# Kernel optimization log

Measured on AMD Instinct MI355X. Metric: run time of the kernel, lower is better.

## Reference

```python
import jax, jax.numpy as jnp
import numpy as np

N_NODES = 50000
N_EDGES = 800000
IN_FEATS = 128
OUT_FEATS = 128
HEADS = 2
EW_DIMS = 2
NEG_SLOPE = 0.2


def setup_inputs() -> dict:
    key = jax.random.key(0)
    ks = jax.random.split(key, 8)
    feat = jax.random.normal(ks[0], (N_NODES, IN_FEATS), dtype=jnp.float32)
    e_w = jax.random.uniform(ks[1], (N_EDGES, EW_DIMS), dtype=jnp.float32)
    src = jax.random.randint(ks[2], (N_EDGES,), 0, N_NODES)
    dst = jax.random.randint(ks[3], (N_EDGES,), 0, N_NODES)
    # Learned params: per-head fc weight, attn vectors (xavier-ish scale)
    s = 1.0 / np.sqrt(IN_FEATS)
    W = jax.random.normal(ks[4], (HEADS, OUT_FEATS, IN_FEATS), dtype=jnp.float32) * s
    attn_l = jax.random.normal(ks[5], (HEADS, OUT_FEATS), dtype=jnp.float32) * s
    attn_r = jax.random.normal(ks[6], (HEADS, OUT_FEATS), dtype=jnp.float32) * s
    attn_ew = jax.random.normal(ks[7], (HEADS, EW_DIMS), dtype=jnp.float32)
    return {"feat": feat, "e_w": e_w, "src": src, "dst": dst,
            "W": W, "attn_l": attn_l, "attn_r": attn_r, "attn_ew": attn_ew}


def reference(feat, e_w, src, dst, W, attn_l, attn_r, attn_ew):
    N = feat.shape[0]
    # per-head projection: [N, H, O]
    ft = jnp.einsum('nf,hof->nho', feat, W)
    el = jnp.einsum('nho,ho->nh', ft, attn_l)           # [N, H]
    er = jnp.einsum('nho,ho->nh', ft, attn_r)           # [N, H]
    ew = jnp.einsum('ed,hd->eh', e_w, attn_ew)          # [E, H]
    # u_add_v + edge-weight attention + leaky_relu
    e = jax.nn.leaky_relu(el[src] + er[dst] + ew, NEG_SLOPE)  # [E, H]
    # edge_softmax grouped by destination node (numerically stable)
    emax = jax.ops.segment_max(e, dst, num_segments=N)
    emax = jnp.where(jnp.isfinite(emax), emax, 0.0)
    ee = jnp.exp(e - emax[dst])
    denom = jax.ops.segment_sum(ee, dst, num_segments=N)
    a = ee / jnp.where(denom[dst] > 0, denom[dst], 1.0)       # [E, H]
    # u_mul_e / sum aggregation: [N, H, O]
    m = ft[src] * a[:, :, None]
    rst = jax.ops.segment_sum(m, dst, num_segments=N)
    # residual (Identity since in_feats == out_feats) + elu, then cat heads
    rst = jax.nn.elu(rst + feat[:, None, :])
    return rst.reshape(N, -1)
```

## Files before the change

### kernel.cpp

```cpp
#include <hip/hip_runtime.h>
#include <math.h>

#define NNODES 50000
#define NEDGES 800000
#define INF 128
#define OUTF 128
#define HEADS 2
#define NEG_SLOPE 0.2f

#define NXCD 8
#define SCAPX 8
#define NSLOT 64
#define DCAP 32
#define OVFCAP 32768
#define OVFFLAG 0x40000000

__device__ __forceinline__ unsigned short f2bf(float f) {
    unsigned u = __float_as_uint(f);
    unsigned r = (u + 0x7FFFu + ((u >> 16) & 1u)) >> 16;
    return (unsigned short)r;
}
__device__ __forceinline__ float bf2f(unsigned short b) {
    return __uint_as_float((unsigned)b << 16);
}
__device__ __forceinline__ unsigned cvt_pk_bf16(float lo, float hi) {
    unsigned r;
    asm("v_cvt_pk_bf16_f32 %0, %1, %2" : "=v"(r) : "v"(lo), "v"(hi));
    return r;
}

typedef __attribute__((ext_vector_type(8))) short frag_ab;
typedef __attribute__((ext_vector_type(4))) float frag_cd;
typedef __attribute__((ext_vector_type(8))) unsigned short ushort8v;

#define APITCH 136

__global__ void init_kernel(int* cur8, int* ,
                            const float* __restrict__ W,
                            const float* __restrict__ attn_l,
                            const float* __restrict__ attn_r,
                            unsigned short* __restrict__ Wb,
                            float* __restrict__ wfold, int N) {
    const int b = blockIdx.x, t = threadIdx.x;
    const int zn = NXCD * N + 1;
    const int zblk = (zn + 255) >> 8;
    if (b < zblk) {
        int i = b * 256 + t;
        if (i < zn) cur8[i] = 0;
        return;
    }
    if (b == zblk) {
        int h = t >> 7, f = t & 127;
        float sl = 0.f, sr = 0.f;
#pragma unroll 16
        for (int o = 0; o < 128; ++o) {
            float wv = W[(size_t)(h * 128 + o) * 128 + f];
            sl = fmaf(attn_l[h * 128 + o], wv, sl);
            sr = fmaf(attn_r[h * 128 + o], wv, sr);
        }
        wfold[h * 128 + f] = sl;
        wfold[(2 + h) * 128 + f] = sr;
        return;
    }
    int base = (b - zblk - 1) * 4096 + t * 16;
#pragma unroll
    for (int q = 0; q < 4; ++q) {
        float4 g = *(const float4*)(W + base + q * 4);
        ushort4 v; v.x = f2bf(g.x); v.y = f2bf(g.y); v.z = f2bf(g.z); v.w = f2bf(g.w);
        *(ushort4*)(Wb + base + q * 4) = v;
    }
}

__global__ __launch_bounds__(256) void gemm_mfma(const float* __restrict__ feat,
                                                 const unsigned short* __restrict__ Wb,
                                                 const float* __restrict__ wfold,
                                                 unsigned short* __restrict__ ftb,
                                                 float* __restrict__ el,
                                                 float* __restrict__ er,
                                                 int N) {
    __shared__ unsigned short Bs[256 * APITCH];
    const int t = threadIdx.x;
    const int w = t >> 6, lane = t & 63;
    const int m16 = lane & 15, quad = lane >> 4;
    const int n0 = blockIdx.x * 128;
    const int r0 = n0 + w * 16 + m16;
    const int r1 = r0 + 64;
    const bool v0 = r0 < N, v1 = r1 < N;

#pragma unroll
    for (int i = 0; i < 16; ++i) {
        int q = t + i * 256;
        int row = q >> 4, c = q & 15;
        ushort8v v = *(const ushort8v*)(Wb + row * 128 + c * 8);
        *(ushort8v*)(&Bs[row * APITCH + c * 8]) = v;
    }

    frag_ab af[2][4];
    float pd[2][4] = {{0.f, 0.f, 0.f, 0.f}, {0.f, 0.f, 0.f, 0.f}};
#pragma unroll
    for (int kc = 0; kc < 4; ++kc) {
        const int cc = kc * 32 + quad * 8;
        float4 ga0 = make_float4(0.f, 0.f, 0.f, 0.f), ga1 = ga0;
        float4 gb0 = ga0, gb1 = ga0;
        if (v0) {
            ga0 = *(const float4*)(feat + (size_t)r0 * INF + cc);
            ga1 = *(const float4*)(feat + (size_t)r0 * INF + cc + 4);
        }
        if (v1) {
            gb0 = *(const float4*)(feat + (size_t)r1 * INF + cc);
            gb1 = *(const float4*)(feat + (size_t)r1 * INF + cc + 4);
        }
        union { int4 i; frag_ab f; } ua, ub;
        ua.i.x = (int)cvt_pk_bf16(ga0.x, ga0.y); ua.i.y = (int)cvt_pk_bf16(ga0.z, ga0.w);
        ua.i.z = (int)cvt_pk_bf16(ga1.x, ga1.y); ua.i.w = (int)cvt_pk_bf16(ga1.z, ga1.w);
        ub.i.x = (int)cvt_pk_bf16(gb0.x, gb0.y); ub.i.y = (int)cvt_pk_bf16(gb0.z, gb0.w);
        ub.i.z = (int)cvt_pk_bf16(gb1.x, gb1.y); ub.i.w = (int)cvt_pk_bf16(gb1.z, gb1.w);
        af[0][kc] = ua.f; af[1][kc] = ub.f;
#pragma unroll
        for (int vq = 0; vq < 4; ++vq) {
            float4 w0 = *(const float4*)(wfold + vq * 128 + cc);
            float4 w1 = *(const float4*)(wfold + vq * 128 + cc + 4);
            pd[0][vq] += ga0.x * w0.x + ga0.y * w0.y + ga0.z * w0.z + ga0.w * w0.w
                       + ga1.x * w1.x + ga1.y * w1.y + ga1.z * w1.z + ga1.w * w1.w;
            pd[1][vq] += gb0.x * w0.x + gb0.y * w0.y + gb0.z * w0.z + gb0.w * w0.w
                       + gb1.x * w1.x + gb1.y * w1.y + gb1.z * w1.z + gb1.w * w1.w;
        }
    }
#pragma unroll
    for (int m = 16; m < 64; m <<= 1)
#pragma unroll
        for (int rg = 0; rg < 2; ++rg)
#pragma unroll
            for (int vq = 0; vq < 4; ++vq) pd[rg][vq] += __shfl_xor(pd[rg][vq], m, 64);
    if (quad == 0) {
        if (v0) {
            *(float2*)(el + (size_t)r0 * 2) = make_float2(pd[0][0], pd[0][1]);
            *(float2*)(er + (size_t)r0 * 2) = make_float2(pd[0][2], pd[0][3]);
        }
        if (v1) {
            *(float2*)(el + (size_t)r1 * 2) = make_float2(pd[1][0], pd[1][1]);
            *(float2*)(er + (size_t)r1 * 2) = make_float2(pd[1][2], pd[1][3]);
        }
    }

    __syncthreads();

#pragma unroll 1
    for (int jt = 0; jt < 4; ++jt) {
        frag_cd acc[2][4];
#pragma unroll
        for (int rg = 0; rg < 2; ++rg)
#pragma unroll
            for (int nt = 0; nt < 4; ++nt) acc[rg][nt] = frag_cd{0.f, 0.f, 0.f, 0.f};
#pragma unroll
        for (int kc = 0; kc < 4; ++kc)
#pragma unroll
            for (int nt = 0; nt < 4; ++nt) {
                frag_ab bf = *(const frag_ab*)(&Bs[(jt * 64 + nt * 16 + m16) * APITCH
                                                   + kc * 32 + quad * 8]);
                acc[0][nt] = __builtin_amdgcn_mfma_f32_16x16x32_bf16(bf, af[0][kc],
                                                                     acc[0][nt], 0, 0, 0);
                acc[1][nt] = __builtin_amdgcn_mfma_f32_16x16x32_bf16(bf, af[1][kc],
                                                                     acc[1][nt], 0, 0, 0);
            }
#pragma unroll
        for (int rg = 0; rg < 2; ++rg) {
            const int rr = rg ? r1 : r0;
            if (rg ? v1 : v0) {
#pragma unroll
                for (int nt = 0; nt < 4; ++nt) {
                    uint2 p;
                    p.x = cvt_pk_bf16(acc[rg][nt][0], acc[rg][nt][1]);
                    p.y = cvt_pk_bf16(acc[rg][nt][2], acc[rg][nt][3]);
                    *(uint2*)(ftb + (size_t)rr * 256 + jt * 64 + nt * 16 + quad * 4) = p;
                }
            }
        }
    }
}

__global__ __launch_bounds__(256) void edge_fused(const float* __restrict__ el,
                           const float* __restrict__ er,
                           const float* __restrict__ e_w, const int* __restrict__ src,
                           const int* __restrict__ dst, const float* __restrict__ attn_ew,
                           int* __restrict__ cur8, int* __restrict__ ovfcnt,
                           uint2* __restrict__ bins, float4* __restrict__ ovf,
                           int E) {
    int e = blockIdx.x * 256 + threadIdx.x;
    if (e >= E) return;
    unsigned xcc;
    asm volatile("s_getreg_b32 %0, hwreg(HW_REG_XCC_ID)" : "=s"(xcc));
    xcc &= (NXCD - 1);
    int s = src[e], d = dst[e];
    float2 ew2 = *(const float2*)(e_w + (size_t)e * 2);
    float2 elv = *(const float2*)(el + (size_t)s * 2);
    float2 erv = *(const float2*)(er + (size_t)d * 2);
    float v0 = elv.x + erv.x + ew2.x * attn_ew[0] + ew2.y * attn_ew[1];
    float v1 = elv.y + erv.y + ew2.x * attn_ew[2] + ew2.y * attn_ew[3];
    v0 = v0 >= 0.f ? v0 : NEG_SLOPE * v0;
    v1 = v1 >= 0.f ? v1 : NEG_SLOPE * v1;
    float ee0 = __expf(v0);
    float ee1 = __expf(v1);
    int pos = __hip_atomic_fetch_add(cur8 + (size_t)d * NXCD + xcc, 1,
                                     __ATOMIC_RELAXED, __HIP_MEMORY_SCOPE_WORKGROUP);
    if (pos < SCAPX) {
        unsigned pk = ((unsigned)f2bf(ee1) << 16) | (unsigned)f2bf(ee0);
        bins[(size_t)d * NSLOT + xcc * SCAPX + pos] = make_uint2((unsigned)s, pk);
    } else {
        int o = atomicAdd(ovfcnt, 1);
        if (o < OVFCAP)
            ovf[o] = make_float4(__int_as_float(d), __int_as_float(s), ee0, ee1);
    }
}

__global__ __launch_bounds__(256) void compact_bins(uint2* __restrict__ bins,
                                                    const int* __restrict__ cur8,
                                                    int* __restrict__ cntd,
                                                    int* __restrict__ ovfcnt,
                                                    float4* __restrict__ ovf, int N) {
    const int t = threadIdx.x;
    const int w = t >> 6, l = t & 63;
    const int n = blockIdx.x * 4 + w;
    if (n >= N) return;
    const int x = l >> 3, slot = l & 7;
    const int cx = cur8[(size_t)n * NXCD + x];
    uint2 rec = bins[(size_t)n * NSLOT + l];
    const int cxc = cx < SCAPX ? cx : SCAPX;
    const bool valid = slot < cxc;
    unsigned long long mask = __ballot(valid);
    int pos = __popcll(mask & ((1ull << l) - 1ull));
    int tot = __popcll(mask);
    bool oflag = __any(slot == 0 && cx > SCAPX) || (tot > DCAP);
    if (valid) {
        if (pos < DCAP) {
            bins[(size_t)n * NSLOT + pos] = rec;
        } else {
            int o = atomicAdd(ovfcnt, 1);
            if (o < OVFCAP)
                ovf[o] = make_float4(__int_as_float(n), __int_as_float((int)rec.x),
                                     bf2f((unsigned short)(rec.y & 0xFFFFu)),
                                     bf2f((unsigned short)(rec.y >> 16)));
        }
    }
    if (l == 0) cntd[n] = (tot < DCAP ? tot : DCAP) | (oflag ? OVFFLAG : 0);
}

__global__ __launch_bounds__(256) void aggregate(const unsigned short* __restrict__ ftb,
                                                 const float* __restrict__ feat,
                                                 const uint2* __restrict__ bins,
                                                 const int* __restrict__ cntd,
                                                 const int* __restrict__ ovfcnt,
                                                 const float4* __restrict__ ovf,
                                                 float* __restrict__ out, int N) {
    const int t = threadIdx.x;
    const int w = t >> 6, l = t & 63;
    const int n = blockIdx.x * 4 + w;
    if (n >= N) return;
    const int hl = l & 31;
    const int half = l >> 5;
    const int c8 = 8 * hl;
    const int h = hl >> 4;
    const int cw = cntd[n];
    const int cnt = cw & 0xFFFF;
    const uint2* eb = bins + (size_t)n * NSLOT;

    float4 a0 = make_float4(0.f, 0.f, 0.f, 0.f);
    float4 a1 = make_float4(0.f, 0.f, 0.f, 0.f);
    float dn = 0.f;
    const int hm = (cnt + 1) >> 1;
#pragma unroll 8
    for (int i = 0; i < hm; ++i) {
        const int j = 2 * i + half;
        const bool vld = j < cnt;
        uint2 rec = eb[vld ? j : 0];
        float aw = bf2f((unsigned short)(h ? (rec.y >> 16) : (rec.y & 0xFFFFu)));
        float a = vld ? aw : 0.f;
        unsigned su = vld ? rec.x : 0u;
        ushort8v v = *(const ushort8v*)(ftb + (size_t)su * 256 + c8);
        dn += a;
        a0.x = fmaf(a, bf2f(v[0]), a0.x);
        a0.y = fmaf(a, bf2f(v[1]), a0.y);
        a0.z = fmaf(a, bf2f(v[2]), a0.z);
        a0.w = fmaf(a, bf2f(v[3]), a0.w);
        a1.x = fmaf(a, bf2f(v[4]), a1.x);
        a1.y = fmaf(a, bf2f(v[5]), a1.y);
        a1.z = fmaf(a, bf2f(v[6]), a1.z);
        a1.w = fmaf(a, bf2f(v[7]), a1.w);
    }
    a0.x += __shfl_xor(a0.x, 32, 64);
    a0.y += __shfl_xor(a0.y, 32, 64);
    a0.z += __shfl_xor(a0.z, 32, 64);
    a0.w += __shfl_xor(a0.w, 32, 64);
    a1.x += __shfl_xor(a1.x, 32, 64);
    a1.y += __shfl_xor(a1.y, 32, 64);
    a1.z += __shfl_xor(a1.z, 32, 64);
    a1.w += __shfl_xor(a1.w, 32, 64);
    dn += __shfl_xor(dn, 32, 64);

    if (cw & OVFFLAG) {
        int no = *ovfcnt; if (no > OVFCAP) no = OVFCAP;
        for (int i = 0; i < no; ++i) {
            float4 ov = ovf[i];
            if (__float_as_int(ov.x) == n) {
                int s = __float_as_int(ov.y);
                float a = h ? ov.w : ov.z;
                dn += a;
                ushort8v v = *(const ushort8v*)(ftb + (size_t)s * 256 + c8);
                a0.x = fmaf(a, bf2f(v[0]), a0.x);
                a0.y = fmaf(a, bf2f(v[1]), a0.y);
                a0.z = fmaf(a, bf2f(v[2]), a0.z);
                a0.w = fmaf(a, bf2f(v[3]), a0.w);
                a1.x = fmaf(a, bf2f(v[4]), a1.x);
                a1.y = fmaf(a, bf2f(v[5]), a1.y);
                a1.z = fmaf(a, bf2f(v[6]), a1.z);
                a1.w = fmaf(a, bf2f(v[7]), a1.w);
            }
        }
    }
    float inv = dn > 0.f ? 1.0f / dn : 0.f;
    const int cb = c8 + 4 * half;
    float4 av = half ? a1 : a0;
    float4 f4 = *(const float4*)(feat + (size_t)n * INF + (cb & 127));
    float4 r;
    r.x = fmaf(av.x, inv, f4.x);
    r.y = fmaf(av.y, inv, f4.y);
    r.z = fmaf(av.z, inv, f4.z);
    r.w = fmaf(av.w, inv, f4.w);
    r.x = r.x > 0.f ? r.x : expm1f(r.x);
    r.y = r.y > 0.f ? r.y : expm1f(r.y);
    r.z = r.z > 0.f ? r.z : expm1f(r.z);
    r.w = r.w > 0.f ? r.w : expm1f(r.w);
    *(float4*)(out + (size_t)n * 256 + cb) = r;
}

extern "C" void kernel_launch(void* const* d_in, const int* in_sizes, int n_in,
                              void* d_out, int out_size, void* d_ws, size_t ws_size,
                              hipStream_t stream) {
    const float* feat    = (const float*)d_in[0];
    const float* e_w     = (const float*)d_in[1];
    const int*   src     = (const int*)d_in[2];
    const int*   dst     = (const int*)d_in[3];
    const float* W       = (const float*)d_in[4];
    const float* attn_l  = (const float*)d_in[5];
    const float* attn_r  = (const float*)d_in[6];
    const float* attn_ew = (const float*)d_in[7];
    float* out = (float*)d_out;

    const int N = in_sizes[0] / INF;
    const int E = in_sizes[2];

    unsigned short* ftb = (unsigned short*)d_ws;
    uint2*  bins   = (uint2*)(ftb + (size_t)N * 256);
    float*  el     = (float*)(bins + (size_t)N * NSLOT);
    float*  er     = el + (size_t)N * 2;
    float*  wfold  = er + (size_t)N * 2;
    unsigned short* Wb = (unsigned short*)(wfold + 512);
    float4* ovf    = (float4*)(Wb + 32768);
    int*    cur8   = (int*)(ovf + OVFCAP);
    int*    ovfcnt = cur8 + (size_t)NXCD * N;
    int*    cntd   = ovfcnt + 1;

    const int zblk = (NXCD * N + 1 + 255) / 256;
    init_kernel<<<zblk + 9, 256, 0, stream>>>(cur8, ovfcnt, W, attn_l, attn_r, Wb, wfold, N);

    gemm_mfma<<<(N + 127) / 128, 256, 0, stream>>>(feat, Wb, wfold, ftb, el, er, N);

    edge_fused<<<(E + 255) / 256, 256, 0, stream>>>(el, er, e_w, src, dst, attn_ew,
                                                    cur8, ovfcnt, bins, ovf, E);

    compact_bins<<<(N + 3) / 4, 256, 0, stream>>>(bins, cur8, cntd, ovfcnt, ovf, N);

    aggregate<<<(N + 3) / 4, 256, 0, stream>>>(ftb, feat, bins, cntd, ovfcnt, ovf, out, N);
}
```

Baseline: 247.3 us.

## Replace per-XCD bins and compaction pass with two-shard device-scope bins

Per-destination bins are now split into two shards chosen by edge parity. Each shard has its own device-scope atomic cursor and spills to the other shard before falling back to the overflow list. This removes the compact_bins kernel and shrinks the bin array from 64 to 32 slots per node, cutting memory traffic and one launch. In exchange, atomics move from workgroup scope per XCD to device scope, which can raise atomic contention. The aggregate loop is also restructured to batch eight record loads and eight feature gathers ahead of the FMAs, exposing more memory-level parallelism.

```diff
diff --git a/kernel.cpp b/kernel.cpp
--- a/kernel.cpp
+++ b/kernel.cpp
@@ -8,12 +8,9 @@
 #define HEADS 2
 #define NEG_SLOPE 0.2f
 
-#define NXCD 8
-#define SCAPX 8
-#define NSLOT 64
-#define DCAP 32
+#define CAP 32
+#define SCAP 16
 #define OVFCAP 32768
-#define OVFFLAG 0x40000000
 
 __device__ __forceinline__ unsigned short f2bf(float f) {
     unsigned u = __float_as_uint(f);
@@ -35,18 +32,18 @@
 
 #define APITCH 136
 
-__global__ void init_kernel(int* cur8, int* ,
+__global__ void init_kernel(int* cursor, int* ovfcnt,
                             const float* __restrict__ W,
                             const float* __restrict__ attn_l,
                             const float* __restrict__ attn_r,
                             unsigned short* __restrict__ Wb,
                             float* __restrict__ wfold, int N) {
     const int b = blockIdx.x, t = threadIdx.x;
-    const int zn = NXCD * N + 1;
-    const int zblk = (zn + 255) >> 8;
+    const int zblk = (2 * N + 255) >> 8;
     if (b < zblk) {
         int i = b * 256 + t;
-        if (i < zn) cur8[i] = 0;
+        if (i < 2 * N) cursor[i] = 0;
+        if (i == 0) *ovfcnt = 0;
         return;
     }
     if (b == zblk) {
@@ -179,18 +176,14 @@
     }
 }
 
-__global__ __launch_bounds__(256) void edge_fused(const float* __restrict__ el,
-                           const float* __restrict__ er,
+__global__ void edge_fused(const float* __restrict__ el, const float* __restrict__ er,
                            const float* __restrict__ e_w, const int* __restrict__ src,
                            const int* __restrict__ dst, const float* __restrict__ attn_ew,
-                           int* __restrict__ cur8, int* __restrict__ ovfcnt,
-                           uint2* __restrict__ bins, float4* __restrict__ ovf,
-                           int E) {
+                           int* __restrict__ cursor, int* __restrict__ ovfcnt,
+                           uint2* __restrict__ edata, float4* __restrict__ ovf,
+                           int N, int E) {
     int e = blockIdx.x * 256 + threadIdx.x;
     if (e >= E) return;
-    unsigned xcc;
-    asm volatile("s_getreg_b32 %0, hwreg(HW_REG_XCC_ID)" : "=s"(xcc));
-    xcc &= (NXCD - 1);
     int s = src[e], d = dst[e];
     float2 ew2 = *(const float2*)(e_w + (size_t)e * 2);
     float2 elv = *(const float2*)(el + (size_t)s * 2);
@@ -201,54 +194,30 @@
     v1 = v1 >= 0.f ? v1 : NEG_SLOPE * v1;
     float ee0 = __expf(v0);
     float ee1 = __expf(v1);
-    int pos = __hip_atomic_fetch_add(cur8 + (size_t)d * NXCD + xcc, 1,
-                                     __ATOMIC_RELAXED, __HIP_MEMORY_SCOPE_WORKGROUP);
-    if (pos < SCAPX) {
-        unsigned pk = ((unsigned)f2bf(ee1) << 16) | (unsigned)f2bf(ee0);
-        bins[(size_t)d * NSLOT + xcc * SCAPX + pos] = make_uint2((unsigned)s, pk);
+    unsigned pk = ((unsigned)f2bf(ee1) << 16) | (unsigned)f2bf(ee0);
+    uint2 rec = make_uint2((unsigned)s, pk);
+    uint2* bin = edata + (size_t)d * CAP;
+    int sh = e & 1;
+    int pos = atomicAdd(cursor + (size_t)sh * N + d, 1);
+    if (pos < SCAP) {
+        bin[sh * SCAP + pos] = rec;
     } else {
-        int o = atomicAdd(ovfcnt, 1);
-        if (o < OVFCAP)
-            ovf[o] = make_float4(__int_as_float(d), __int_as_float(s), ee0, ee1);
-    }
-}
-
-__global__ __launch_bounds__(256) void compact_bins(uint2* __restrict__ bins,
-                                                    const int* __restrict__ cur8,
-                                                    int* __restrict__ cntd,
-                                                    int* __restrict__ ovfcnt,
-                                                    float4* __restrict__ ovf, int N) {
-    const int t = threadIdx.x;
-    const int w = t >> 6, l = t & 63;
-    const int n = blockIdx.x * 4 + w;
-    if (n >= N) return;
-    const int x = l >> 3, slot = l & 7;
-    const int cx = cur8[(size_t)n * NXCD + x];
-    uint2 rec = bins[(size_t)n * NSLOT + l];
-    const int cxc = cx < SCAPX ? cx : SCAPX;
-    const bool valid = slot < cxc;
-    unsigned long long mask = __ballot(valid);
-    int pos = __popcll(mask & ((1ull << l) - 1ull));
-    int tot = __popcll(mask);
-    bool oflag = __any(slot == 0 && cx > SCAPX) || (tot > DCAP);
-    if (valid) {
-        if (pos < DCAP) {
-            bins[(size_t)n * NSLOT + pos] = rec;
+        sh ^= 1;
+        int pos2 = atomicAdd(cursor + (size_t)sh * N + d, 1);
+        if (pos2 < SCAP) {
+            bin[sh * SCAP + pos2] = rec;
         } else {
             int o = atomicAdd(ovfcnt, 1);
             if (o < OVFCAP)
-                ovf[o] = make_float4(__int_as_float(n), __int_as_float((int)rec.x),
-                                     bf2f((unsigned short)(rec.y & 0xFFFFu)),
-                                     bf2f((unsigned short)(rec.y >> 16)));
-        }
-    }
-    if (l == 0) cntd[n] = (tot < DCAP ? tot : DCAP) | (oflag ? OVFFLAG : 0);
+                ovf[o] = make_float4(__int_as_float(d), __int_as_float(s), ee0, ee1);
+        }
+    }
 }
 
 __global__ __launch_bounds__(256) void aggregate(const unsigned short* __restrict__ ftb,
                                                  const float* __restrict__ feat,
-                                                 const uint2* __restrict__ bins,
-                                                 const int* __restrict__ cntd,
+                                                 const uint2* __restrict__ edata,
+                                                 const int* __restrict__ cursor,
                                                  const int* __restrict__ ovfcnt,
                                                  const float4* __restrict__ ovf,
                                                  float* __restrict__ out, int N) {
@@ -260,32 +229,44 @@
     const int half = l >> 5;
     const int c8 = 8 * hl;
     const int h = hl >> 4;
-    const int cw = cntd[n];
-    const int cnt = cw & 0xFFFF;
-    const uint2* eb = bins + (size_t)n * NSLOT;
+    const int c0c = cursor[n], c1c = cursor[N + n];
+    const int cnt0 = c0c < SCAP ? c0c : SCAP;
+    const int cnt1 = c1c < SCAP ? c1c : SCAP;
+    const int cnt = cnt0 + cnt1;
+    const uint2* eb = edata + (size_t)n * CAP;
+    const unsigned short* ftbc = ftb + c8;
 
     float4 a0 = make_float4(0.f, 0.f, 0.f, 0.f);
     float4 a1 = make_float4(0.f, 0.f, 0.f, 0.f);
     float dn = 0.f;
     const int hm = (cnt + 1) >> 1;
-#pragma unroll 8
-    for (int i = 0; i < hm; ++i) {
-        const int j = 2 * i + half;
-        const bool vld = j < cnt;
-        uint2 rec = eb[vld ? j : 0];
-        float aw = bf2f((unsigned short)(h ? (rec.y >> 16) : (rec.y & 0xFFFFu)));
-        float a = vld ? aw : 0.f;
-        unsigned su = vld ? rec.x : 0u;
-        ushort8v v = *(const ushort8v*)(ftb + (size_t)su * 256 + c8);
-        dn += a;
-        a0.x = fmaf(a, bf2f(v[0]), a0.x);
-        a0.y = fmaf(a, bf2f(v[1]), a0.y);
-        a0.z = fmaf(a, bf2f(v[2]), a0.z);
-        a0.w = fmaf(a, bf2f(v[3]), a0.w);
-        a1.x = fmaf(a, bf2f(v[4]), a1.x);
-        a1.y = fmaf(a, bf2f(v[5]), a1.y);
-        a1.z = fmaf(a, bf2f(v[6]), a1.z);
-        a1.w = fmaf(a, bf2f(v[7]), a1.w);
+    for (int cb = 0; cb < hm; cb += 8) {
+        uint2 rc[8];
+#pragma unroll
+        for (int k = 0; k < 8; ++k) {
+            const int j = 2 * (cb + k) + half;
+            const bool vld = j < cnt;
+            const int jj = j < cnt0 ? j : j - cnt0 + SCAP;
+            rc[k] = vld ? eb[jj] : make_uint2(0u, 0u);
+        }
+        ushort8v vv[8];
+#pragma unroll
+        for (int k = 0; k < 8; ++k)
+            vv[k] = *(const ushort8v*)(ftbc + (size_t)rc[k].x * 256);
+#pragma unroll
+        for (int k = 0; k < 8; ++k) {
+            const float a = bf2f((unsigned short)(h ? (rc[k].y >> 16)
+                                                    : (rc[k].y & 0xFFFFu)));
+            dn += a;
+            a0.x = fmaf(a, bf2f(vv[k][0]), a0.x);
+            a0.y = fmaf(a, bf2f(vv[k][1]), a0.y);
+            a0.z = fmaf(a, bf2f(vv[k][2]), a0.z);
+            a0.w = fmaf(a, bf2f(vv[k][3]), a0.w);
+            a1.x = fmaf(a, bf2f(vv[k][4]), a1.x);
+            a1.y = fmaf(a, bf2f(vv[k][5]), a1.y);
+            a1.z = fmaf(a, bf2f(vv[k][6]), a1.z);
+            a1.w = fmaf(a, bf2f(vv[k][7]), a1.w);
+        }
     }
     a0.x += __shfl_xor(a0.x, 32, 64);
     a0.y += __shfl_xor(a0.y, 32, 64);
@@ -297,7 +278,7 @@
     a1.w += __shfl_xor(a1.w, 32, 64);
     dn += __shfl_xor(dn, 32, 64);
 
-    if (cw & OVFFLAG) {
+    if (c0c > SCAP && c1c > SCAP) {
         int no = *ovfcnt; if (no > OVFCAP) no = OVFCAP;
         for (int i = 0; i < no; ++i) {
             float4 ov = ovf[i];
@@ -318,9 +299,9 @@
         }
     }
     float inv = dn > 0.f ? 1.0f / dn : 0.f;
-    const int cb = c8 + 4 * half;
+    const int cb2 = c8 + 4 * half;
     float4 av = half ? a1 : a0;
-    float4 f4 = *(const float4*)(feat + (size_t)n * INF + (cb & 127));
+    float4 f4 = *(const float4*)(feat + (size_t)n * INF + (cb2 & 127));
     float4 r;
     r.x = fmaf(av.x, inv, f4.x);
     r.y = fmaf(av.y, inv, f4.y);
@@ -330,7 +311,7 @@
     r.y = r.y > 0.f ? r.y : expm1f(r.y);
     r.z = r.z > 0.f ? r.z : expm1f(r.z);
     r.w = r.w > 0.f ? r.w : expm1f(r.w);
-    *(float4*)(out + (size_t)n * 256 + cb) = r;
+    *(float4*)(out + (size_t)n * 256 + cb2) = r;
 }
 
 extern "C" void kernel_launch(void* const* d_in, const int* in_sizes, int n_in,
@@ -350,25 +331,22 @@
     const int E = in_sizes[2];
 
     unsigned short* ftb = (unsigned short*)d_ws;
-    uint2*  bins   = (uint2*)(ftb + (size_t)N * 256);
-    float*  el     = (float*)(bins + (size_t)N * NSLOT);
+    uint2*  edata  = (uint2*)(ftb + (size_t)N * 256);
+    float*  el     = (float*)(edata + (size_t)N * CAP);
     float*  er     = el + (size_t)N * 2;
     float*  wfold  = er + (size_t)N * 2;
     unsigned short* Wb = (unsigned short*)(wfold + 512);
     float4* ovf    = (float4*)(Wb + 32768);
-    int*    cur8   = (int*)(ovf + OVFCAP);
-    int*    ovfcnt = cur8 + (size_t)NXCD * N;
-    int*    cntd   = ovfcnt + 1;
-
-    const int zblk = (NXCD * N + 1 + 255) / 256;
-    init_kernel<<<zblk + 9, 256, 0, stream>>>(cur8, ovfcnt, W, attn_l, attn_r, Wb, wfold, N);
+    int*    cursor = (int*)(ovf + OVFCAP);
+    int*    ovfcnt = cursor + 2 * (size_t)N;
+
+    const int zblk = (2 * N + 255) / 256;
+    init_kernel<<<zblk + 9, 256, 0, stream>>>(cursor, ovfcnt, W, attn_l, attn_r, Wb, wfold, N);
 
     gemm_mfma<<<(N + 127) / 128, 256, 0, stream>>>(feat, Wb, wfold, ftb, el, er, N);
 
     edge_fused<<<(E + 255) / 256, 256, 0, stream>>>(el, er, e_w, src, dst, attn_ew,
-                                                    cur8, ovfcnt, bins, ovf, E);
-
-    compact_bins<<<(N + 3) / 4, 256, 0, stream>>>(bins, cur8, cntd, ovfcnt, ovf, N);
-
-    aggregate<<<(N + 3) / 4, 256, 0, stream>>>(ftb, feat, bins, cntd, ovfcnt, ovf, out, N);
-}
+                                                    cursor, ovfcnt, edata, ovf, N, E);
+
+    aggregate<<<(N + 3) / 4, 256, 0, stream>>>(ftb, feat, edata, cursor, ovfcnt, ovf, out, N);
+}
```

Result: faster. 232.3 us (-6.1%).
